# Kernel tuning notes

Measured on AMD Instinct MI355X. Metric: run time of the kernel, lower is better.

Reference implementation:

```python
import jax, jax.numpy as jnp
import numpy as np

MARGIN = 0.5
SCALE = 64.0

N, D, C, S = 512, 512, 100000, 1


def setup_inputs() -> dict:
    key = jax.random.key(0)
    k1, k2, k3 = jax.random.split(key, 3)
    emb = jax.random.normal(k1, (N, D), dtype=jnp.float32)
    # Real face pipelines feed L2-normalized embeddings; also keeps acos well-conditioned.
    emb = emb / jnp.linalg.norm(emb, axis=1, keepdims=True)
    w = jax.random.normal(k2, (D, C, S), dtype=jnp.float32)
    labels = jax.random.randint(k3, (N,), 0, C)
    target = jax.nn.one_hot(labels, C, dtype=jnp.float32)  # [N, C]
    return {"embedding_batch": emb, "w_param": w, "target_batch": target}


def reference(embedding_batch, w_param, target_batch):
    # normalize class centers over the embedding dim (dim=0 of w)
    w_n = w_param / jnp.linalg.norm(w_param, axis=0, keepdims=True)  # [D, C, S]
    # cosine similarities via GEMM instead of broadcast mult-reduce: [N, C, S]
    cos = jnp.einsum('nd,dcs->ncs', embedding_batch, w_n)
    cos = jnp.clip(cos, -1.0, 1.0)
    cos = jnp.max(cos, axis=2)                    # best subclass -> [N, C]
    theta = jnp.arccos(cos)                       # [N, C]
    logits = jnp.cos(theta + target_batch * MARGIN) * SCALE
    # faithful to the original: softmax over dim=0 (the batch axis)
    return jax.nn.softmax(logits, axis=0)
```

## Files before the change

kernel.cpp:

```cpp
#include <hip/hip_runtime.h>
#include <hip/hip_bf16.h>


static constexpr int DIM    = 512;
static constexpr int NROWS  = 512;
static constexpr int NCLS   = 100000;
static constexpr int BC     = 64;
static constexpr int BK     = 32;
static constexpr int NSTEP  = DIM / BK;
static constexpr int MT     = NROWS / 16;
static constexpr int NBLK   = (NCLS + BC - 1) / BC;
static constexpr int WTBLK  = NBLK * 2;

static constexpr float COS_M = 0.87758256189037271611f;
static constexpr float SIN_M = 0.47942553860420300027f;
static constexpr float SCALE = 64.0f;
static constexpr float SHIFT = 20.0f;

typedef __attribute__((ext_vector_type(8))) short bf16x8;
typedef __attribute__((ext_vector_type(4))) float f32x4;

#define MFMA16(A, B, C) __builtin_amdgcn_mfma_f32_16x16x32_bf16((A), (B), (C), 0, 0, 0)

__device__ __forceinline__ unsigned short f2bf(float f) {
  union { float f; unsigned u; } v; v.f = f;
  unsigned u = v.u;
  return (unsigned short)((u + 0x7FFFu + ((u >> 16) & 1u)) >> 16);
}

__global__ __launch_bounds__(1024)
void label_scan(const float* __restrict__ tgt, int* __restrict__ labels) {
  const int row = blockIdx.x;
  const int nq = NCLS / 4;
  const int q0 = blockIdx.y * (nq / 4);
  const int q1 = (blockIdx.y == 3) ? nq : q0 + (nq / 4);
  const float4* rp = reinterpret_cast<const float4*>(tgt + (size_t)row * NCLS);
  int found = -1;
  for (int c4 = q0 + threadIdx.x; c4 < q1; c4 += 1024) {
    const float4 v = rp[c4];
    if (v.x > 0.5f) found = c4 * 4 + 0;
    if (v.y > 0.5f) found = c4 * 4 + 1;
    if (v.z > 0.5f) found = c4 * 4 + 2;
    if (v.w > 0.5f) found = c4 * 4 + 3;
  }
  if (found >= 0) labels[row] = found;
}

__global__ void prep_afrag(const float* __restrict__ emb,
                           unsigned short* __restrict__ afrag) {
  const int idx = blockIdx.x * blockDim.x + threadIdx.x;
  const int l  = idx & 63;
  const int mt = (idx >> 6) & 31;
  const int ks = idx >> 11;
  const int row = mt * 16 + (l & 15);
  const int k0  = ks * 32 + (l >> 4) * 8;

  unsigned short t[8];
#pragma unroll
  for (int j = 0; j < 8; ++j) t[j] = f2bf(emb[row * DIM + k0 + j]);

  uint4 v;
  v.x = (unsigned)t[0] | ((unsigned)t[1] << 16);
  v.y = (unsigned)t[2] | ((unsigned)t[3] << 16);
  v.z = (unsigned)t[4] | ((unsigned)t[5] << 16);
  v.w = (unsigned)t[6] | ((unsigned)t[7] << 16);
  *reinterpret_cast<uint4*>(&afrag[(size_t)idx * 8]) = v;
}

__global__ __launch_bounds__(256)
void wt_kernel(const float* __restrict__ w,
               unsigned short* __restrict__ bfrag,
               float* __restrict__ rnorm) {
  __shared__ float S[32][33];
  __shared__ float NRM[32][32];

  const int t  = threadIdx.x;
  const int cb = blockIdx.x;
  const int c0 = cb * 32;
  const bool valid = c0 < NCLS;

  const int rk = t >> 3;
  const int rc = (t & 7) * 4;

  float4 nrm4 = {0.f, 0.f, 0.f, 0.f};

  for (int p = 0; p < NSTEP; ++p) {
    float4 v = {0.f, 0.f, 0.f, 0.f};
    if (valid)
      v = *reinterpret_cast<const float4*>(w + (size_t)(p * BK + rk) * NCLS + c0 + rc);
    nrm4.x += v.x * v.x; nrm4.y += v.y * v.y;
    nrm4.z += v.z * v.z; nrm4.w += v.w * v.w;
    __syncthreads();
    *reinterpret_cast<float4*>(&S[rk][rc]) = v;
    __syncthreads();

    if (t < 128) {
      const int l2 = t & 63;
      const int j  = t >> 6;
      const int col = j * 16 + (l2 & 15);
      const int kb  = (l2 >> 4) * 8;
      uint4 pk;
      pk.x = (unsigned)f2bf(S[kb + 0][col]) | ((unsigned)f2bf(S[kb + 1][col]) << 16);
      pk.y = (unsigned)f2bf(S[kb + 2][col]) | ((unsigned)f2bf(S[kb + 3][col]) << 16);
      pk.z = (unsigned)f2bf(S[kb + 4][col]) | ((unsigned)f2bf(S[kb + 5][col]) << 16);
      pk.w = (unsigned)f2bf(S[kb + 6][col]) | ((unsigned)f2bf(S[kb + 7][col]) << 16);
      *reinterpret_cast<uint4*>(
          &bfrag[(((size_t)(cb * NSTEP + p) * 2 + j) * 64 + l2) * 8]) = pk;
    }
  }

  NRM[rk][rc + 0] = nrm4.x;
  NRM[rk][rc + 1] = nrm4.y;
  NRM[rk][rc + 2] = nrm4.z;
  NRM[rk][rc + 3] = nrm4.w;
  __syncthreads();
  if (t < 32) {
    float s = 0.f;
#pragma unroll
    for (int g = 0; g < 32; ++g) s += NRM[g][t];
    rnorm[c0 + t] = rsqrtf(fmaxf(s, 1e-20f));
  }
}

__global__ __launch_bounds__(1024, 4)
void arcface_main(const unsigned short* __restrict__ bfrag,
                  const unsigned short* __restrict__ afrag,
                  const float* __restrict__ rnorm,
                  const int* __restrict__ labels,
                  float* __restrict__ out) {
  __shared__ alignas(16) unsigned short B2[2][2048];
  __shared__ float red[16][BC];
  __shared__ float colv[BC];

  const int tid = threadIdx.x;
  const int wv  = tid >> 6;
  const int l   = tid & 63;
  const int lh  = l >> 4;
  const int ll  = l & 15;
  const int c0  = blockIdx.x * BC;
  const int cb0 = blockIdx.x * 2;

  const char* bfb  = (const char*)bfrag;
  const char* aptr = (const char*)afrag + (size_t)(wv * 2) * 1024 + (size_t)l * 16;
  char* b2b = (char*)&B2[0][0];

  f32x4 acc[2][4] = {};
  bf16x8 a2[2][2];

#define STAGE(KS, BUF)                                                          \
  if (wv < 4) {                                                                 \
    const int dof = __builtin_amdgcn_readfirstlane((BUF) * 4096 + wv * 1024);   \
    __builtin_amdgcn_global_load_lds(                                           \
        (const __attribute__((address_space(1))) void*)                        \
            (bfb + (size_t)((cb0 + (wv >> 1)) * 32 + (KS) * 2 + (wv & 1)) * 1024 \
                 + (size_t)l * 16),                                             \
        (__attribute__((address_space(3))) void*)(b2b + dof), 16, 0, 0);        \
  }

  STAGE(0, 0)
  a2[0][0] = *reinterpret_cast<const bf16x8*>(aptr + 0);
  a2[0][1] = *reinterpret_cast<const bf16x8*>(aptr + 1024);
  STAGE(1, 1)

#define STEP(KS, VMS)                                                           \
  {                                                                             \
    if (wv < 4) { asm volatile("s_waitcnt vmcnt(" #VMS ")" ::: "memory"); }     \
    else        { asm volatile("s_waitcnt vmcnt(0)" ::: "memory"); }            \
    __builtin_amdgcn_s_barrier();                                               \
    __builtin_amdgcn_sched_barrier(0);                                          \
    bf16x8 b0 = *reinterpret_cast<const bf16x8*>(b2b + ((KS) & 1) * 4096 + 0 * 1024 + l * 16); \
    bf16x8 b1 = *reinterpret_cast<const bf16x8*>(b2b + ((KS) & 1) * 4096 + 1 * 1024 + l * 16); \
    bf16x8 b2 = *reinterpret_cast<const bf16x8*>(b2b + ((KS) & 1) * 4096 + 2 * 1024 + l * 16); \
    bf16x8 b3 = *reinterpret_cast<const bf16x8*>(b2b + ((KS) & 1) * 4096 + 3 * 1024 + l * 16); \
    if ((KS) + 1 < NSTEP) {                                                     \
      a2[((KS) + 1) & 1][0] =                                                   \
          *reinterpret_cast<const bf16x8*>(aptr + (size_t)((KS) + 1) * 32768);  \
      a2[((KS) + 1) & 1][1] =                                                   \
          *reinterpret_cast<const bf16x8*>(aptr + (size_t)((KS) + 1) * 32768 + 1024); \
    }                                                                           \
    asm volatile("s_waitcnt lgkmcnt(0)" ::: "memory");                          \
    __builtin_amdgcn_sched_barrier(0);                                          \
    __builtin_amdgcn_s_barrier();                                               \
    if ((KS) + 2 < NSTEP) STAGE((KS) + 2, (KS) & 1)                             \
    __builtin_amdgcn_sched_barrier(0);                                          \
    acc[0][0] = MFMA16(a2[(KS) & 1][0], b0, acc[0][0]);                         \
    acc[0][1] = MFMA16(a2[(KS) & 1][0], b1, acc[0][1]);                         \
    acc[0][2] = MFMA16(a2[(KS) & 1][0], b2, acc[0][2]);                         \
    acc[0][3] = MFMA16(a2[(KS) & 1][0], b3, acc[0][3]);                         \
    acc[1][0] = MFMA16(a2[(KS) & 1][1], b0, acc[1][0]);                         \
    acc[1][1] = MFMA16(a2[(KS) & 1][1], b1, acc[1][1]);                         \
    acc[1][2] = MFMA16(a2[(KS) & 1][1], b2, acc[1][2]);                         \
    acc[1][3] = MFMA16(a2[(KS) & 1][1], b3, acc[1][3]);                         \
  }

  STEP(0, 1)   STEP(1, 1)   STEP(2, 1)   STEP(3, 1)
  STEP(4, 1)   STEP(5, 1)   STEP(6, 1)   STEP(7, 1)
  STEP(8, 1)   STEP(9, 1)   STEP(10, 1)  STEP(11, 1)
  STEP(12, 1)  STEP(13, 1)  STEP(14, 1)  STEP(15, 0)
#undef STEP
#undef STAGE

  float rn[4];
#pragma unroll
  for (int jj = 0; jj < 4; ++jj) rn[jj] = rnorm[c0 + jj * 16 + ll];

  int lab[2][4];
#pragma unroll
  for (int i = 0; i < 2; ++i)
#pragma unroll
    for (int q = 0; q < 4; ++q)
      lab[i][q] = labels[wv * 32 + i * 16 + lh * 4 + q];

  float sme[4] = {0.f, 0.f, 0.f, 0.f};
#pragma unroll
  for (int jj = 0; jj < 4; ++jj) {
    const int cj = c0 + jj * 16 + ll;
#pragma unroll
    for (int i = 0; i < 2; ++i) {
#pragma unroll
      for (int q = 0; q < 4; ++q) {
        float cosv = acc[i][jj][q] * rn[jj];
        cosv = fminf(fmaxf(cosv, -1.f), 1.f);
        float lg;
        if (lab[i][q] == cj) {
          const float s = sqrtf(fmaxf(1.f - cosv * cosv, 0.f));
          lg = cosv * COS_M - s * SIN_M;
        } else {
          lg = cosv;
        }
        const float e = __expf(lg * SCALE - SHIFT);
        acc[i][jj][q] = e;
        sme[jj] += e;
      }
    }
  }

#pragma unroll
  for (int jj = 0; jj < 4; ++jj) {
    sme[jj] += __shfl_xor(sme[jj], 16, 64);
    sme[jj] += __shfl_xor(sme[jj], 32, 64);
  }
  if (l < 16) {
#pragma unroll
    for (int jj = 0; jj < 4; ++jj) red[wv][jj * 16 + l] = sme[jj];
  }
  __syncthreads();
  if (tid < BC) {
    float s = 0.f;
#pragma unroll
    for (int v2 = 0; v2 < 16; ++v2) s += red[v2][tid];
    colv[tid] = s;
  }
  __syncthreads();

#pragma unroll
  for (int jj = 0; jj < 4; ++jj) {
    const int cj = c0 + jj * 16 + ll;
    if (cj >= NCLS) continue;
    const float rs = 1.0f / colv[jj * 16 + ll];
#pragma unroll
    for (int i = 0; i < 2; ++i) {
#pragma unroll
      for (int q = 0; q < 4; ++q) {
        const int row = wv * 32 + i * 16 + lh * 4 + q;
        out[(size_t)row * NCLS + cj] = acc[i][jj][q] * rs;
      }
    }
  }
}

extern "C" void kernel_launch(void* const* d_in, const int* in_sizes, int n_in,
                              void* d_out, int out_size, void* d_ws, size_t ws_size,
                              hipStream_t stream) {
  const float* emb = (const float*)d_in[0];
  const float* w   = (const float*)d_in[1];
  const float* tgt = (const float*)d_in[2];
  float* out = (float*)d_out;

  char* ws = (char*)d_ws;
  int* labels           = (int*)ws;
  unsigned short* afrag = (unsigned short*)(ws + 4096);
  float* rnorm          = (float*)(ws + (1u << 20));
  unsigned short* bfrag = (unsigned short*)(ws + (2u << 20));

  label_scan<<<dim3(NROWS, 4), 1024, 0, stream>>>(tgt, labels);
  prep_afrag<<<64, 512, 0, stream>>>(emb, afrag);
  wt_kernel<<<WTBLK, 256, 0, stream>>>(w, bfrag, rnorm);
  arcface_main<<<NBLK, 1024, 0, stream>>>(bfrag, afrag, rnorm, labels, out);
}
```

Baseline: 274.4 us.

## Halve class tile to 32 and use triple-buffered LDS with one barrier per step

Shrinks the per-block class tile from 64 to 32 columns, doubling the number of blocks and raising the occupancy hint to 8 blocks per CU. The B-fragment staging moves from double to triple buffering, which removes the second barrier in each k-step because the buffer being refilled is never the one being read. It also drops the padding and bounds checks, since 100000 divides evenly by 32. The cost is half as many MFMAs per LDS load and the A fragments being reloaded across twice as many blocks, which raises global traffic for the shared embedding operand.

Result: faster. 269.0 us (-2.0%).

```diff
diff --git a/kernel.cpp b/kernel.cpp
--- a/kernel.cpp
+++ b/kernel.cpp
@@ -5,12 +5,11 @@
 static constexpr int DIM    = 512;
 static constexpr int NROWS  = 512;
 static constexpr int NCLS   = 100000;
-static constexpr int BC     = 64;
+static constexpr int BC     = 32;
 static constexpr int BK     = 32;
 static constexpr int NSTEP  = DIM / BK;
 static constexpr int MT     = NROWS / 16;
-static constexpr int NBLK   = (NCLS + BC - 1) / BC;
-static constexpr int WTBLK  = NBLK * 2;
+static constexpr int NBLK   = NCLS / BC;
 
 static constexpr float COS_M = 0.87758256189037271611f;
 static constexpr float SIN_M = 0.47942553860420300027f;
@@ -77,7 +76,6 @@
   const int t  = threadIdx.x;
   const int cb = blockIdx.x;
   const int c0 = cb * 32;
-  const bool valid = c0 < NCLS;
 
   const int rk = t >> 3;
   const int rc = (t & 7) * 4;
@@ -85,9 +83,8 @@
   float4 nrm4 = {0.f, 0.f, 0.f, 0.f};
 
   for (int p = 0; p < NSTEP; ++p) {
-    float4 v = {0.f, 0.f, 0.f, 0.f};
-    if (valid)
-      v = *reinterpret_cast<const float4*>(w + (size_t)(p * BK + rk) * NCLS + c0 + rc);
+    const float4 v = *reinterpret_cast<const float4*>(
+        w + (size_t)(p * BK + rk) * NCLS + c0 + rc);
     nrm4.x += v.x * v.x; nrm4.y += v.y * v.y;
     nrm4.z += v.z * v.z; nrm4.w += v.w * v.w;
     __syncthreads();
@@ -122,13 +119,13 @@
   }
 }
 
-__global__ __launch_bounds__(1024, 4)
+__global__ __launch_bounds__(1024, 8)
 void arcface_main(const unsigned short* __restrict__ bfrag,
                   const unsigned short* __restrict__ afrag,
                   const float* __restrict__ rnorm,
                   const int* __restrict__ labels,
                   float* __restrict__ out) {
-  __shared__ alignas(16) unsigned short B2[2][2048];
+  __shared__ alignas(16) unsigned short B3[3][1024];
   __shared__ float red[16][BC];
   __shared__ float colv[BC];
 
@@ -138,23 +135,21 @@
   const int lh  = l >> 4;
   const int ll  = l & 15;
   const int c0  = blockIdx.x * BC;
-  const int cb0 = blockIdx.x * 2;
-
-  const char* bfb  = (const char*)bfrag;
+
+  const char* bfb  = (const char*)bfrag + (size_t)blockIdx.x * 32768;
   const char* aptr = (const char*)afrag + (size_t)(wv * 2) * 1024 + (size_t)l * 16;
-  char* b2b = (char*)&B2[0][0];
-
-  f32x4 acc[2][4] = {};
+  char* b3b = (char*)&B3[0][0];
+
+  f32x4 acc[2][2] = {};
   bf16x8 a2[2][2];
 
 #define STAGE(KS, BUF)                                                          \
-  if (wv < 4) {                                                                 \
-    const int dof = __builtin_amdgcn_readfirstlane((BUF) * 4096 + wv * 1024);   \
+  if (wv < 2) {                                                                 \
+    const int dof = __builtin_amdgcn_readfirstlane((BUF) * 2048 + wv * 1024);   \
     __builtin_amdgcn_global_load_lds(                                           \
         (const __attribute__((address_space(1))) void*)                        \
-            (bfb + (size_t)((cb0 + (wv >> 1)) * 32 + (KS) * 2 + (wv & 1)) * 1024 \
-                 + (size_t)l * 16),                                             \
-        (__attribute__((address_space(3))) void*)(b2b + dof), 16, 0, 0);        \
+            (bfb + (size_t)((KS) * 2 + wv) * 1024 + (size_t)l * 16),            \
+        (__attribute__((address_space(3))) void*)(b3b + dof), 16, 0, 0);        \
   }
 
   STAGE(0, 0)
@@ -164,14 +159,12 @@
 
 #define STEP(KS, VMS)                                                           \
   {                                                                             \
-    if (wv < 4) { asm volatile("s_waitcnt vmcnt(" #VMS ")" ::: "memory"); }     \
+    if (wv < 2) { asm volatile("s_waitcnt vmcnt(" #VMS ")" ::: "memory"); }     \
     else        { asm volatile("s_waitcnt vmcnt(0)" ::: "memory"); }            \
     __builtin_amdgcn_s_barrier();                                               \
     __builtin_amdgcn_sched_barrier(0);                                          \
-    bf16x8 b0 = *reinterpret_cast<const bf16x8*>(b2b + ((KS) & 1) * 4096 + 0 * 1024 + l * 16); \
-    bf16x8 b1 = *reinterpret_cast<const bf16x8*>(b2b + ((KS) & 1) * 4096 + 1 * 1024 + l * 16); \
-    bf16x8 b2 = *reinterpret_cast<const bf16x8*>(b2b + ((KS) & 1) * 4096 + 2 * 1024 + l * 16); \
-    bf16x8 b3 = *reinterpret_cast<const bf16x8*>(b2b + ((KS) & 1) * 4096 + 3 * 1024 + l * 16); \
+    bf16x8 b0 = *reinterpret_cast<const bf16x8*>(b3b + ((KS) % 3) * 2048 + l * 16);        \
+    bf16x8 b1 = *reinterpret_cast<const bf16x8*>(b3b + ((KS) % 3) * 2048 + 1024 + l * 16); \
     if ((KS) + 1 < NSTEP) {                                                     \
       a2[((KS) + 1) & 1][0] =                                                   \
           *reinterpret_cast<const bf16x8*>(aptr + (size_t)((KS) + 1) * 32768);  \
@@ -180,17 +173,11 @@
     }                                                                           \
     asm volatile("s_waitcnt lgkmcnt(0)" ::: "memory");                          \
     __builtin_amdgcn_sched_barrier(0);                                          \
-    __builtin_amdgcn_s_barrier();                                               \
-    if ((KS) + 2 < NSTEP) STAGE((KS) + 2, (KS) & 1)                             \
-    __builtin_amdgcn_sched_barrier(0);                                          \
+    if ((KS) + 2 < NSTEP) STAGE((KS) + 2, ((KS) + 2) % 3)                       \
     acc[0][0] = MFMA16(a2[(KS) & 1][0], b0, acc[0][0]);                         \
     acc[0][1] = MFMA16(a2[(KS) & 1][0], b1, acc[0][1]);                         \
-    acc[0][2] = MFMA16(a2[(KS) & 1][0], b2, acc[0][2]);                         \
-    acc[0][3] = MFMA16(a2[(KS) & 1][0], b3, acc[0][3]);                         \
     acc[1][0] = MFMA16(a2[(KS) & 1][1], b0, acc[1][0]);                         \
     acc[1][1] = MFMA16(a2[(KS) & 1][1], b1, acc[1][1]);                         \
-    acc[1][2] = MFMA16(a2[(KS) & 1][1], b2, acc[1][2]);                         \
-    acc[1][3] = MFMA16(a2[(KS) & 1][1], b3, acc[1][3]);                         \
   }
 
   STEP(0, 1)   STEP(1, 1)   STEP(2, 1)   STEP(3, 1)
@@ -200,9 +187,9 @@
 #undef STEP
 #undef STAGE
 
-  float rn[4];
-#pragma unroll
-  for (int jj = 0; jj < 4; ++jj) rn[jj] = rnorm[c0 + jj * 16 + ll];
+  float rn[2];
+#pragma unroll
+  for (int j = 0; j < 2; ++j) rn[j] = rnorm[c0 + j * 16 + ll];
 
   int lab[2][4];
 #pragma unroll
@@ -211,15 +198,15 @@
     for (int q = 0; q < 4; ++q)
       lab[i][q] = labels[wv * 32 + i * 16 + lh * 4 + q];
 
-  float sme[4] = {0.f, 0.f, 0.f, 0.f};
-#pragma unroll
-  for (int jj = 0; jj < 4; ++jj) {
-    const int cj = c0 + jj * 16 + ll;
+  float sme[2] = {0.f, 0.f};
+#pragma unroll
+  for (int j = 0; j < 2; ++j) {
+    const int cj = c0 + j * 16 + ll;
 #pragma unroll
     for (int i = 0; i < 2; ++i) {
 #pragma unroll
       for (int q = 0; q < 4; ++q) {
-        float cosv = acc[i][jj][q] * rn[jj];
+        float cosv = acc[i][j][q] * rn[j];
         cosv = fminf(fmaxf(cosv, -1.f), 1.f);
         float lg;
         if (lab[i][q] == cj) {
@@ -229,20 +216,21 @@
           lg = cosv;
         }
         const float e = __expf(lg * SCALE - SHIFT);
-        acc[i][jj][q] = e;
-        sme[jj] += e;
+        acc[i][j][q] = e;
+        sme[j] += e;
       }
     }
   }
 
 #pragma unroll
-  for (int jj = 0; jj < 4; ++jj) {
-    sme[jj] += __shfl_xor(sme[jj], 16, 64);
-    sme[jj] += __shfl_xor(sme[jj], 32, 64);
-  }
+  for (int j = 0; j < 2; ++j) {
+    sme[j] += __shfl_xor(sme[j], 16, 64);
+    sme[j] += __shfl_xor(sme[j], 32, 64);
+  }
+  __syncthreads();
   if (l < 16) {
 #pragma unroll
-    for (int jj = 0; jj < 4; ++jj) red[wv][jj * 16 + l] = sme[jj];
+    for (int j = 0; j < 2; ++j) red[wv][j * 16 + l] = sme[j];
   }
   __syncthreads();
   if (tid < BC) {
@@ -253,17 +241,19 @@
   }
   __syncthreads();
 
-#pragma unroll
-  for (int jj = 0; jj < 4; ++jj) {
-    const int cj = c0 + jj * 16 + ll;
-    if (cj >= NCLS) continue;
-    const float rs = 1.0f / colv[jj * 16 + ll];
+  float rs[2];
+#pragma unroll
+  for (int j = 0; j < 2; ++j) rs[j] = 1.0f / colv[j * 16 + ll];
+
+#pragma unroll
+  for (int j = 0; j < 2; ++j) {
+    const int cj = c0 + j * 16 + ll;
 #pragma unroll
     for (int i = 0; i < 2; ++i) {
 #pragma unroll
       for (int q = 0; q < 4; ++q) {
         const int row = wv * 32 + i * 16 + lh * 4 + q;
-        out[(size_t)row * NCLS + cj] = acc[i][jj][q] * rs;
+        out[(size_t)row * NCLS + cj] = acc[i][j][q] * rs[j];
       }
     }
   }
@@ -285,6 +275,6 @@
 
   label_scan<<<dim3(NROWS, 4), 1024, 0, stream>>>(tgt, labels);
   prep_afrag<<<64, 512, 0, stream>>>(emb, afrag);
-  wt_kernel<<<WTBLK, 256, 0, stream>>>(w, bfrag, rnorm);
+  wt_kernel<<<NBLK, 256, 0, stream>>>(w, bfrag, rnorm);
   arcface_main<<<NBLK, 1024, 0, stream>>>(bfrag, afrag, rnorm, labels, out);
 }
```
